# Kernel tuning notes

Measured on AMD Instinct MI355X. Metric: run time of the kernel, lower is better.

The kernel has to match this reference:

```python
import jax, jax.numpy as jnp
import numpy as np

B, N, D_IN, D_OUT, NHOP = 16, 1024, 128, 128, 3


def setup_inputs() -> dict:
    key = jax.random.key(0)
    ks = jax.random.split(key, 7)
    x = jax.random.normal(ks[0], (B, N, D_IN), dtype=jnp.float32)
    # sparse-ish binary adjacency (float, as in the torch model) with self loops
    adj = (jax.random.uniform(ks[1], (B, N, N)) < 0.05).astype(jnp.float32)
    adj = jnp.maximum(adj, jnp.eye(N, dtype=jnp.float32)[None])
    # learned params (torch nn.Linear default-ish init scale)
    s_in = 1.0 / np.sqrt(D_IN)
    s_out = 1.0 / np.sqrt(2 * D_OUT)
    W_w = jax.random.uniform(ks[2], (D_OUT, D_IN), minval=-s_in, maxval=s_in, dtype=jnp.float32)
    W_b = jax.random.uniform(ks[3], (D_OUT,), minval=-s_in, maxval=s_in, dtype=jnp.float32)
    A = jax.random.normal(ks[4], (D_OUT, D_OUT), dtype=jnp.float32) * 0.02  # nn.Parameter(zeros) would kill signal; use small init
    gate_w = jax.random.uniform(ks[5], (1, 2 * D_OUT), minval=-s_out, maxval=s_out, dtype=jnp.float32)
    gate_b = jax.random.uniform(ks[6], (1,), minval=-s_out, maxval=s_out, dtype=jnp.float32)
    return {"x": x, "adj": adj, "W_w": W_w, "W_b": W_b, "A": A,
            "gate_w": gate_w, "gate_b": gate_b}


def reference(x, adj, W_w, W_b, A, gate_w, gate_b):
    # h = W(x): [B,N,D_OUT]
    h = jnp.einsum('bnd,od->bno', x, W_w) + W_b
    # bilinear score e[b,j,k] = (h A)_j . h_k, symmetrized
    e = jnp.einsum('bjl,bkl->bjk', jnp.einsum('bjd,de->bje', h, A), h)
    e = e + jnp.swapaxes(e, 1, 2)
    # masked softmax over dim=1 (as in the torch code), then re-mask
    att = jnp.where(adj > 0, e, jnp.zeros((), dtype=e.dtype))
    att = jax.nn.softmax(att, axis=1)
    att = att * adj
    retval = h
    for _ in range(NHOP):
        az = jax.nn.relu(jnp.einsum('bij,bjk->bik', att, retval))
        gate_in = jnp.concatenate([h, az], axis=-1)            # [B,N,2*D_OUT]
        coeff = jax.nn.sigmoid(jnp.einsum('bnf,of->bno', gate_in, gate_w) + gate_b)  # [B,N,1]
        retval = coeff * h + (1.0 - coeff) * az
    return retval
```

## Files before the change

kernel.cpp:

```cpp
#include <hip/hip_runtime.h>
#include <math.h>

#define Bn 16
#define Nn 1024
#define Dn 128

typedef unsigned short ushort;
typedef unsigned long long u64;
typedef short short8 __attribute__((ext_vector_type(8)));
typedef float f32x4 __attribute__((ext_vector_type(4)));
typedef ushort us8 __attribute__((ext_vector_type(8)));
typedef ushort us4 __attribute__((ext_vector_type(4)));

__device__ __forceinline__ ushort f2bf(float f) {
    unsigned u = __float_as_uint(f);
    u += 0x7fff + ((u >> 16) & 1);
    return (ushort)(u >> 16);
}
__device__ __forceinline__ float bf2f(ushort s) {
    return __uint_as_float(((unsigned)s) << 16);
}

#if defined(__has_builtin)
#if __has_builtin(__builtin_amdgcn_global_load_lds)
#define HAVE_GLL 1
#endif
#endif
#ifndef HAVE_GLL
#define HAVE_GLL 0
#endif

typedef __attribute__((address_space(1))) void as1_t;
typedef __attribute__((address_space(3))) void as3_t;

__device__ __forceinline__ void stage_group(const void* gbase, void* lbase, int lane) {
#if HAVE_GLL
    __builtin_amdgcn_global_load_lds((as1_t*)((const char*)gbase + lane * 16),
                                     (as3_t*)lbase, 16, 0, 0);
#else
    *(us8*)((char*)lbase + lane * 16) = *(const us8*)((const char*)gbase + lane * 16);
#endif
}


__global__ __launch_bounds__(256) void k_ph0(const float* __restrict__ Ww,
                                             const float* __restrict__ A,
                                             const float* __restrict__ adj,
                                             ushort* __restrict__ Whi, ushort* __restrict__ Wlo,
                                             ushort* __restrict__ AThi, ushort* __restrict__ ATlo,
                                             float* __restrict__ Z, u64* __restrict__ bm) {
    int L = blockIdx.x, t = threadIdx.x;
    if (L < 64) {
        int i = L * 256 + t;
        float w = Ww[i];
        ushort wh = f2bf(w);
        Whi[i] = wh;
        Wlo[i] = f2bf(w - bf2f(wh));
        int e = i >> 7, d = i & 127;
        float a = A[d * Dn + e];
        ushort ah = f2bf(a);
        AThi[i] = ah;
        ATlo[i] = f2bf(a - bf2f(ah));
        Z[i] = (float)Nn;
    }
    int gwv = L * 4 + (t >> 6);
    int lane = t & 63;
    #pragma unroll 4
    for (int it = 0; it < 16; ++it) {
        int pair = gwv * 16 + it;
        const float* p = adj + (size_t)pair * 256 + lane * 4;
        float4 v = *(const float4*)p;
        u64 b0 = __ballot(v.x > 0.f);
        u64 b1 = __ballot(v.y > 0.f);
        u64 b2 = __ballot(v.z > 0.f);
        u64 b3 = __ballot(v.w > 0.f);
        if (lane == 0) {
            u64* d = bm + (size_t)pair * 4;
            d[0] = b0; d[1] = b1; d[2] = b2; d[3] = b3;
        }
    }
}

__global__ __launch_bounds__(256) void k_h(const float* __restrict__ x,
                                           const float* __restrict__ Wb,
                                           const ushort* __restrict__ Whi,
                                           const ushort* __restrict__ Wlo,
                                           const ushort* __restrict__ AThi,
                                           const ushort* __restrict__ ATlo,
                                           float* __restrict__ h,
                                           ushort* __restrict__ h16f,
                                           ushort* __restrict__ hA16f) {
    int I0 = blockIdx.x * 16;
    int t = threadIdx.x, w = t >> 6, lane = t & 63;
    int m = lane & 15, q = lane >> 4;

    __shared__ float xs[16][Dn + 4];
    __shared__ float hs[16][Dn + 4];
    __shared__ float has[16][Dn + 4];

    {
        int r = t >> 4, c8 = (t & 15) * 8;
        const float* src = x + (size_t)(I0 + r) * Dn + c8;
        *(float4*)&xs[r][c8]     = *(const float4*)(src);
        *(float4*)&xs[r][c8 + 4] = *(const float4*)(src + 4);
    }
    __syncthreads();

    f32x4 acc0 = {0,0,0,0}, acc1 = {0,0,0,0};
    #pragma unroll
    for (int ks = 0; ks < 4; ++ks) {
        int k0 = q * 8 + ks * 32;
        float v[8]; short8 ahi, alo;
        *(float4*)(v)     = *(const float4*)(&xs[m][k0]);
        *(float4*)(v + 4) = *(const float4*)(&xs[m][k0 + 4]);
        #pragma unroll
        for (int j = 0; j < 8; ++j) {
            ushort hi = f2bf(v[j]);
            ahi[j] = (short)hi;
            alo[j] = (short)f2bf(v[j] - bf2f(hi));
        }
        #pragma unroll
        for (int nn = 0; nn < 2; ++nn) {
            int brow = (w * 2 + nn) * 16 + m;
            short8 bhi = __builtin_bit_cast(short8, ((const us8*)(Whi + (size_t)brow * Dn))[q + ks * 4]);
            short8 blo = __builtin_bit_cast(short8, ((const us8*)(Wlo + (size_t)brow * Dn))[q + ks * 4]);
            f32x4 acc = nn ? acc1 : acc0;
            acc = __builtin_amdgcn_mfma_f32_16x16x32_bf16(ahi, bhi, acc, 0, 0, 0);
            acc = __builtin_amdgcn_mfma_f32_16x16x32_bf16(alo, bhi, acc, 0, 0, 0);
            acc = __builtin_amdgcn_mfma_f32_16x16x32_bf16(ahi, blo, acc, 0, 0, 0);
            if (nn) acc1 = acc; else acc0 = acc;
        }
    }
    #pragma unroll
    for (int nn = 0; nn < 2; ++nn) {
        int col = (w * 2 + nn) * 16 + m;
        float bias = Wb[col];
        f32x4 acc = nn ? acc1 : acc0;
        #pragma unroll
        for (int r = 0; r < 4; ++r) {
            int rl = q * 4 + r;
            float hv = acc[r] + bias;
            h[(size_t)(I0 + rl) * Dn + col] = hv;
            hs[rl][col] = hv;
        }
    }
    __syncthreads();

    f32x4 bcc0 = {0,0,0,0}, bcc1 = {0,0,0,0};
    #pragma unroll
    for (int ks = 0; ks < 4; ++ks) {
        int k0 = q * 8 + ks * 32;
        float v[8]; short8 ahi, alo;
        *(float4*)(v)     = *(const float4*)(&hs[m][k0]);
        *(float4*)(v + 4) = *(const float4*)(&hs[m][k0 + 4]);
        #pragma unroll
        for (int j = 0; j < 8; ++j) {
            ushort hi = f2bf(v[j]);
            ahi[j] = (short)hi;
            alo[j] = (short)f2bf(v[j] - bf2f(hi));
        }
        #pragma unroll
        for (int nn = 0; nn < 2; ++nn) {
            int brow = (w * 2 + nn) * 16 + m;
            short8 bhi = __builtin_bit_cast(short8, ((const us8*)(AThi + (size_t)brow * Dn))[q + ks * 4]);
            short8 blo = __builtin_bit_cast(short8, ((const us8*)(ATlo + (size_t)brow * Dn))[q + ks * 4]);
            f32x4 acc = nn ? bcc1 : bcc0;
            acc = __builtin_amdgcn_mfma_f32_16x16x32_bf16(ahi, bhi, acc, 0, 0, 0);
            acc = __builtin_amdgcn_mfma_f32_16x16x32_bf16(alo, bhi, acc, 0, 0, 0);
            acc = __builtin_amdgcn_mfma_f32_16x16x32_bf16(ahi, blo, acc, 0, 0, 0);
            if (nn) bcc1 = acc; else bcc0 = acc;
        }
    }
    #pragma unroll
    for (int nn = 0; nn < 2; ++nn) {
        int col = (w * 2 + nn) * 16 + m;
        f32x4 acc = nn ? bcc1 : bcc0;
        #pragma unroll
        for (int r = 0; r < 4; ++r)
            has[q * 4 + r][col] = acc[r];
    }
    __syncthreads();

    {
        int kc = t >> 6, mm = (t >> 2) & 15, qq = t & 3;
        int cb = kc * 32 + qq * 8;
        us8 oh, oa;
        #pragma unroll
        for (int e = 0; e < 8; ++e) {
            oh[e] = f2bf(hs[mm][cb + e]);
            oa[e] = f2bf(has[mm][cb + e]);
        }
        size_t U = (size_t)(I0 >> 4) * 256 + kc * 64 + mm * 4 + qq;
        ((us8*)h16f)[U]  = oh;
        ((us8*)hA16f)[U] = oa;
    }
}

__global__ __launch_bounds__(256, 2) void k_scores(const ushort* __restrict__ h16f,
                                                   const ushort* __restrict__ hA16f,
                                                   const u64* __restrict__ bm,
                                                   ushort* __restrict__ Ef,
                                                   float* __restrict__ Z) {
    int L = blockIdx.x;
    int b    = ((L & 7) << 1) | (L >> 11);
    int tile = (L >> 3) & 255;
    int I0 = (tile >> 4) << 6;
    int J0 = (tile & 15) << 6;
    int t = threadIdx.x, wid = t >> 6, lane = t & 63;
    int m = lane & 15, q = lane >> 4;

    __shared__ __align__(16) char smem[66560];
    float (*sc)[68] = (float(*)[68])smem;
    float (*cz)[64] = (float(*)[64])(smem + 65536);

    {
        const char* hb  = (const char*)h16f  + (size_t)b * 16384 * 16;
        const char* ab  = (const char*)hA16f + (size_t)b * 16384 * 16;
        for (int g = wid; g < 64; g += 4) {
            int arr = g >> 4, rt_l = (g >> 2) & 3, kk = g & 3;
            int rbase = ((arr < 2) ? (I0 >> 4) : (J0 >> 4)) + rt_l;
            const char* base = (arr & 1) ? ab : hb;
            const char* gp = base + ((size_t)rbase * 256 + kk * 64) * 16;
            stage_group(gp, smem + g * 1024, lane);
        }
    }
    __syncthreads();

    int off16 = (m * 4 + q) * 16;
    f32x4 acc[4] = {};
    #pragma unroll
    for (int ks = 0; ks < 4; ++ks) {
        short8 a1 = __builtin_bit_cast(short8, *(const us8*)(smem + 16384 + (wid * 4 + ks) * 1024 + off16));
        short8 a2 = __builtin_bit_cast(short8, *(const us8*)(smem +         (wid * 4 + ks) * 1024 + off16));
        #pragma unroll
        for (int nt = 0; nt < 4; ++nt) {
            short8 b1 = __builtin_bit_cast(short8, *(const us8*)(smem + 32768 + (nt * 4 + ks) * 1024 + off16));
            short8 b2 = __builtin_bit_cast(short8, *(const us8*)(smem + 49152 + (nt * 4 + ks) * 1024 + off16));
            acc[nt] = __builtin_amdgcn_mfma_f32_16x16x32_bf16(a1, b1, acc[nt], 0, 0, 0);
            acc[nt] = __builtin_amdgcn_mfma_f32_16x16x32_bf16(a2, b2, acc[nt], 0, 0, 0);
        }
    }
    __syncthreads();

    #pragma unroll
    for (int nt = 0; nt < 4; ++nt)
        #pragma unroll
        for (int r = 0; r < 4; ++r)
            sc[wid * 16 + q * 4 + r][nt * 16 + m] = acc[nt][r];
    __syncthreads();

    int row16 = t >> 4, c = t & 15;
    int bitc = ((J0 >> 2) & 63) + c;
    float colsum[4] = {0.f, 0.f, 0.f, 0.f};
    #pragma unroll
    for (int it = 0; it < 4; ++it) {
        int row = it * 16 + row16;
        const u64* wp = bm + ((size_t)(b * Nn + I0 + row) * 4 + (J0 >> 8)) * 4;
        u64 wj[4] = {wp[0], wp[1], wp[2], wp[3]};
        float s4[4];
        *(float4*)s4 = *(const float4*)(&sc[row][c * 4]);
        us4 e4;
        #pragma unroll
        for (int j = 0; j < 4; ++j) {
            float ex = __expf(s4[j]);
            bool on = (wj[j] >> bitc) & 1;
            e4[j] = f2bf(on ? ex : 0.f);
            colsum[j] += on ? (ex - 1.0f) : 0.f;
        }
        size_t U = ((((size_t)b * 64 + (I0 >> 4) + it) * 32 + (J0 >> 5) + (c >> 3)) * 16 + row16) * 4
                 + ((c & 7) >> 1);
        *(us4*)(Ef + U * 8 + (c & 1) * 4) = e4;
    }
    #pragma unroll
    for (int j = 0; j < 4; ++j) {
        colsum[j] += __shfl_xor(colsum[j], 16, 64);
        colsum[j] += __shfl_xor(colsum[j], 32, 64);
    }
    if (lane < 16) {
        #pragma unroll
        for (int j = 0; j < 4; ++j) cz[wid][lane * 4 + j] = colsum[j];
    }
    __syncthreads();
    if (t < 64) {
        float s = cz[0][t] + cz[1][t] + cz[2][t] + cz[3][t];
        atomicAdd(&Z[b * Nn + J0 + t], s);
    }
}

__global__ __launch_bounds__(256) void k_prep(const float* __restrict__ src,
                                              const float* __restrict__ Z,
                                              ushort* __restrict__ Tf) {
    int b = blockIdx.y;
    int j0 = blockIdx.x * 64;
    int t = threadIdx.x;
    __shared__ float ls[64][129];
    __shared__ float iz[64];
    if (t < 64) iz[t] = 1.0f / Z[b * Nn + j0 + t];
    __syncthreads();
    #pragma unroll
    for (int it = 0; it < 8; ++it) {
        int idx = it * 256 + t;
        int j = idx >> 5, k4 = (idx & 31) * 4;
        float4 v = *(const float4*)(src + ((size_t)b * Nn + j0 + j) * Dn + k4);
        float z = iz[j];
        ls[j][k4] = v.x * z; ls[j][k4 + 1] = v.y * z;
        ls[j][k4 + 2] = v.z * z; ls[j][k4 + 3] = v.w * z;
    }
    __syncthreads();
    int k = t & 127, half = t >> 7;
    us8 o[4];
    #pragma unroll
    for (int qq = 0; qq < 4; ++qq) {
        us8 tmp;
        #pragma unroll
        for (int e = 0; e < 8; ++e)
            tmp[e] = f2bf(ls[half * 32 + qq * 8 + e][k]);
        o[qq] = tmp;
    }
    size_t U = (((size_t)(k >> 4) * 32 + (j0 >> 5) + half) * 16 + (k & 15)) * 4;
    us8* dst = (us8*)(Tf + (size_t)b * 131072 + U * 8);
    dst[0] = o[0]; dst[1] = o[1]; dst[2] = o[2]; dst[3] = o[3];
}

__global__ __launch_bounds__(256) void k_hop(const ushort* __restrict__ Ef,
                                             const ushort* __restrict__ Tf,
                                             const float* __restrict__ h,
                                             const float* __restrict__ Z,
                                             const float* __restrict__ gw,
                                             const float* __restrict__ gb,
                                             ushort* __restrict__ Tfn,
                                             float* __restrict__ out,
                                             int last) {
    int L = blockIdx.x;
    int b  = ((L & 7) << 1) | (L >> 7);
    int t4 = (L >> 3) & 15;
    int t = threadIdx.x, w = t >> 6, lane = t & 63;
    int m = lane & 15, q = lane >> 4;
    int rt = t4 * 4 + w;
    int I0 = rt << 4;

    __shared__ __align__(16) char smem[49152];
    int off16 = (m * 4 + q) * 16;

    f32x4 acc[8] = {};
    for (int cch = 0; cch < 8; ++cch) {
        for (int g = w; g < 48; g += 4) {
            const char* gp; char* lp;
            if (g < 16) {
                int rr = g >> 2, kk = g & 3;
                gp = (const char*)Ef + ((((size_t)b * 64 + t4 * 4 + rr) * 32 + cch * 4 + kk) * 64) * 16;
                lp = smem + g * 1024;
            } else {
                int gb2 = g - 16, nt = gb2 >> 2, kk = gb2 & 3;
                gp = (const char*)Tf + ((((size_t)b * 8 + nt) * 32 + cch * 4 + kk) * 64) * 16;
                lp = smem + 16384 + gb2 * 1024;
            }
            stage_group(gp, lp, lane);
        }
        __syncthreads();

        #pragma unroll
        for (int kk = 0; kk < 4; ++kk) {
            short8 a = __builtin_bit_cast(short8, *(const us8*)(smem + (w * 4 + kk) * 1024 + off16));
            #pragma unroll
            for (int nt = 0; nt < 8; ++nt) {
                short8 bf = __builtin_bit_cast(short8,
                    *(const us8*)(smem + 16384 + (nt * 4 + kk) * 1024 + off16));
                acc[nt] = __builtin_amdgcn_mfma_f32_16x16x32_bf16(a, bf, acc[nt], 0, 0, 0);
            }
        }
        __syncthreads();
    }

    float gb0 = gb[0];
    float gwa[8], gwz[8];
    #pragma unroll
    for (int nt = 0; nt < 8; ++nt) { gwa[nt] = gw[nt * 16 + m]; gwz[nt] = gw[Dn + nt * 16 + m]; }

    float hv[8][4], coef[4];
    size_t hbase = ((size_t)b * Nn + I0) * Dn;
    #pragma unroll
    for (int r = 0; r < 4; ++r) {
        int row = q * 4 + r;
        float gs = 0.f;
        #pragma unroll
        for (int nt = 0; nt < 8; ++nt) {
            float az = fmaxf(acc[nt][r], 0.f);
            acc[nt][r] = az;
            float hh = h[hbase + (size_t)row * Dn + nt * 16 + m];
            hv[nt][r] = hh;
            gs += hh * gwa[nt] + az * gwz[nt];
        }
        gs += __shfl_xor(gs, 1, 64);
        gs += __shfl_xor(gs, 2, 64);
        gs += __shfl_xor(gs, 4, 64);
        gs += __shfl_xor(gs, 8, 64);
        coef[r] = 1.0f / (1.0f + __expf(-(gs + gb0)));
    }

    if (last) {
        #pragma unroll
        for (int r = 0; r < 4; ++r) {
            int row = q * 4 + r;
            float cc = coef[r];
            #pragma unroll
            for (int nt = 0; nt < 8; ++nt)
                out[hbase + (size_t)row * Dn + nt * 16 + m] =
                    cc * hv[nt][r] + (1.f - cc) * acc[nt][r];
        }
    } else {
        ushort (*tt)[128][16] = (ushort(*)[128][16])smem;
        #pragma unroll
        for (int r = 0; r < 4; ++r) {
            int row = q * 4 + r;
            float cc = coef[r];
            float iz = 1.0f / Z[b * Nn + I0 + row];
            #pragma unroll
            for (int nt = 0; nt < 8; ++nt) {
                float v = cc * hv[nt][r] + (1.f - cc) * acc[nt][r];
                tt[w][nt * 16 + m][row] = f2bf(v * iz);
            }
        }
        __syncthreads();
        int k = t >> 1, jh = t & 1;
        size_t U0 = (((size_t)(k >> 4) * 32 + t4 * 2 + jh) * 16 + (k & 15)) * 4;
        ushort* dst = Tfn + (size_t)b * 131072 + U0 * 8;
        #pragma unroll
        for (int qq = 0; qq < 4; ++qq)
            *(us8*)(dst + qq * 8) = *(const us8*)&tt[jh * 2 + (qq >> 1)][k][(qq & 1) * 8];
    }
}

extern "C" void kernel_launch(void* const* d_in, const int* in_sizes, int n_in,
                              void* d_out, int out_size, void* d_ws, size_t ws_size,
                              hipStream_t stream) {
    const float* x    = (const float*)d_in[0];
    const float* adj  = (const float*)d_in[1];
    const float* Ww   = (const float*)d_in[2];
    const float* Wb   = (const float*)d_in[3];
    const float* A    = (const float*)d_in[4];
    const float* gw   = (const float*)d_in[5];
    const float* gb   = (const float*)d_in[6];
    float* out = (float*)d_out;

    char* ws = (char*)d_ws;
    float*  h    = (float*)(ws);
    ushort* Ta   = (ushort*)(ws + (8u << 20));
    ushort* Tb   = (ushort*)(ws + (12u << 20));
    ushort* E    = (ushort*)(ws + (16u << 20));
    float*  Z    = (float*)(ws + (48u << 20));
    ushort* Whi  = (ushort*)(ws + (48u << 20) + (64u << 10));
    ushort* Wlo  = (ushort*)(ws + (48u << 20) + (96u << 10));
    ushort* AThi = (ushort*)(ws + (48u << 20) + (128u << 10));
    ushort* ATlo = (ushort*)(ws + (48u << 20) + (160u << 10));
    u64*    bm   = (u64*)(ws + (48u << 20) + (192u << 10));

    k_ph0   <<<1024, 256, 0, stream>>>(Ww, A, adj, Whi, Wlo, AThi, ATlo, Z, bm);
    k_h     <<<1024, 256, 0, stream>>>(x, Wb, Whi, Wlo, AThi, ATlo, h, Ta, Tb);
    k_scores<<<4096, 256, 0, stream>>>(Ta, Tb, bm, E, Z);
    k_prep  <<<dim3(16, Bn), 256, 0, stream>>>(h, Z, Ta);
    k_hop   <<<256, 256, 0, stream>>>(E, Ta, h, Z, gw, gb, Tb, out, 0);
    k_hop   <<<256, 256, 0, stream>>>(E, Tb, h, Z, gw, gb, Ta, out, 0);
    k_hop   <<<256, 256, 0, stream>>>(E, Ta, h, Z, gw, gb, (ushort*)nullptr, out, 1);
}
```

Baseline: 228.9 us.

## Shrink LDS in scores and split hop work across 1024 blocks

k_scores now loads the A-side (row) fragments straight from global memory into registers and stages only the column tiles in LDS. This halves shared memory so four blocks can fit per CU. k_hop is restructured so each block handles one 16-row tile, and its four waves split the 128 output columns instead of the rows. That raises the grid from 256 to 1024 blocks and fills the GPU better. The B operand (T) is now read directly from global memory without LDS staging, and the gate dot product is reduced across waves through shared memory. The cost is more redundant global reads of T across blocks and an extra block synchronisation for the gate reduction.

Result: no change. 231.6 us (+1.2%).

```diff
diff --git a/kernel.cpp b/kernel.cpp
--- a/kernel.cpp
+++ b/kernel.cpp
@@ -196,7 +196,7 @@
     }
 }
 
-__global__ __launch_bounds__(256, 2) void k_scores(const ushort* __restrict__ h16f,
+__global__ __launch_bounds__(256, 4) void k_scores(const ushort* __restrict__ h16f,
                                                    const ushort* __restrict__ hA16f,
                                                    const u64* __restrict__ bm,
                                                    ushort* __restrict__ Ef,
@@ -209,33 +209,44 @@
     int t = threadIdx.x, wid = t >> 6, lane = t & 63;
     int m = lane & 15, q = lane >> 4;
 
-    __shared__ __align__(16) char smem[66560];
+    __shared__ __align__(16) char smem[33792];
     float (*sc)[68] = (float(*)[68])smem;
-    float (*cz)[64] = (float(*)[64])(smem + 65536);
+    float (*cz)[64] = (float(*)[64])(smem + 32768);
 
     {
-        const char* hb  = (const char*)h16f  + (size_t)b * 16384 * 16;
-        const char* ab  = (const char*)hA16f + (size_t)b * 16384 * 16;
-        for (int g = wid; g < 64; g += 4) {
+        const char* hb = (const char*)h16f  + (size_t)b * 16384 * 16;
+        const char* ab = (const char*)hA16f + (size_t)b * 16384 * 16;
+        for (int g = wid; g < 32; g += 4) {
             int arr = g >> 4, rt_l = (g >> 2) & 3, kk = g & 3;
-            int rbase = ((arr < 2) ? (I0 >> 4) : (J0 >> 4)) + rt_l;
-            const char* base = (arr & 1) ? ab : hb;
+            int rbase = (J0 >> 4) + rt_l;
+            const char* base = arr ? ab : hb;
             const char* gp = base + ((size_t)rbase * 256 + kk * 64) * 16;
             stage_group(gp, smem + g * 1024, lane);
         }
     }
-    __syncthreads();
-
-    int off16 = (m * 4 + q) * 16;
+
+    const us8* Hf = (const us8*)h16f  + (size_t)b * 16384;
+    const us8* Af = (const us8*)hA16f + (size_t)b * 16384;
+    int off = m * 4 + q;
+    int rtA = (I0 >> 4) + wid;
+    us8 A1[4], A2[4];
+    #pragma unroll
+    for (int ks = 0; ks < 4; ++ks) {
+        A1[ks] = Af[rtA * 256 + ks * 64 + off];
+        A2[ks] = Hf[rtA * 256 + ks * 64 + off];
+    }
+    __syncthreads();
+
+    int off16 = off * 16;
     f32x4 acc[4] = {};
     #pragma unroll
     for (int ks = 0; ks < 4; ++ks) {
-        short8 a1 = __builtin_bit_cast(short8, *(const us8*)(smem + 16384 + (wid * 4 + ks) * 1024 + off16));
-        short8 a2 = __builtin_bit_cast(short8, *(const us8*)(smem +         (wid * 4 + ks) * 1024 + off16));
+        short8 a1 = __builtin_bit_cast(short8, A1[ks]);
+        short8 a2 = __builtin_bit_cast(short8, A2[ks]);
         #pragma unroll
         for (int nt = 0; nt < 4; ++nt) {
-            short8 b1 = __builtin_bit_cast(short8, *(const us8*)(smem + 32768 + (nt * 4 + ks) * 1024 + off16));
-            short8 b2 = __builtin_bit_cast(short8, *(const us8*)(smem + 49152 + (nt * 4 + ks) * 1024 + off16));
+            short8 b1 = __builtin_bit_cast(short8, *(const us8*)(smem +         (nt * 4 + ks) * 1024 + off16));
+            short8 b2 = __builtin_bit_cast(short8, *(const us8*)(smem + 16384 + (nt * 4 + ks) * 1024 + off16));
             acc[nt] = __builtin_amdgcn_mfma_f32_16x16x32_bf16(a1, b1, acc[nt], 0, 0, 0);
             acc[nt] = __builtin_amdgcn_mfma_f32_16x16x32_bf16(a2, b2, acc[nt], 0, 0, 0);
         }
@@ -322,112 +333,99 @@
     dst[0] = o[0]; dst[1] = o[1]; dst[2] = o[2]; dst[3] = o[3];
 }
 
-__global__ __launch_bounds__(256) void k_hop(const ushort* __restrict__ Ef,
-                                             const ushort* __restrict__ Tf,
-                                             const float* __restrict__ h,
-                                             const float* __restrict__ Z,
-                                             const float* __restrict__ gw,
-                                             const float* __restrict__ gb,
-                                             ushort* __restrict__ Tfn,
-                                             float* __restrict__ out,
-                                             int last) {
+__global__ __launch_bounds__(256, 4) void k_hop(const ushort* __restrict__ Ef,
+                                                const ushort* __restrict__ Tf,
+                                                const float* __restrict__ h,
+                                                const float* __restrict__ Z,
+                                                const float* __restrict__ gw,
+                                                const float* __restrict__ gb,
+                                                ushort* __restrict__ Tfn,
+                                                float* __restrict__ out,
+                                                int last) {
     int L = blockIdx.x;
-    int b  = ((L & 7) << 1) | (L >> 7);
-    int t4 = (L >> 3) & 15;
+    int b  = ((L & 7) << 1) | (L >> 9);
+    int rt = (L >> 3) & 63;
+    int I0 = rt << 4;
     int t = threadIdx.x, w = t >> 6, lane = t & 63;
     int m = lane & 15, q = lane >> 4;
-    int rt = t4 * 4 + w;
-    int I0 = rt << 4;
-
-    __shared__ __align__(16) char smem[49152];
-    int off16 = (m * 4 + q) * 16;
-
-    f32x4 acc[8] = {};
-    for (int cch = 0; cch < 8; ++cch) {
-        for (int g = w; g < 48; g += 4) {
-            const char* gp; char* lp;
-            if (g < 16) {
-                int rr = g >> 2, kk = g & 3;
-                gp = (const char*)Ef + ((((size_t)b * 64 + t4 * 4 + rr) * 32 + cch * 4 + kk) * 64) * 16;
-                lp = smem + g * 1024;
-            } else {
-                int gb2 = g - 16, nt = gb2 >> 2, kk = gb2 & 3;
-                gp = (const char*)Tf + ((((size_t)b * 8 + nt) * 32 + cch * 4 + kk) * 64) * 16;
-                lp = smem + 16384 + gb2 * 1024;
-            }
-            stage_group(gp, lp, lane);
-        }
-        __syncthreads();
-
-        #pragma unroll
-        for (int kk = 0; kk < 4; ++kk) {
-            short8 a = __builtin_bit_cast(short8, *(const us8*)(smem + (w * 4 + kk) * 1024 + off16));
-            #pragma unroll
-            for (int nt = 0; nt < 8; ++nt) {
-                short8 bf = __builtin_bit_cast(short8,
-                    *(const us8*)(smem + 16384 + (nt * 4 + kk) * 1024 + off16));
-                acc[nt] = __builtin_amdgcn_mfma_f32_16x16x32_bf16(a, bf, acc[nt], 0, 0, 0);
-            }
-        }
-        __syncthreads();
+
+    __shared__ __align__(16) char smem[33152];
+    float (*red)[16] = (float(*)[16])(smem + 32768);
+    float* cs = (float*)(smem + 32768 + 256);
+    float* zz = (float*)(smem + 32768 + 320);
+    ushort (*tt)[24] = (ushort(*)[24])smem;
+
+    {
+        const char* Eb = (const char*)Ef + ((size_t)b * 64 + rt) * 32768;
+        for (int g = w; g < 32; g += 4)
+            stage_group(Eb + g * 1024, smem + g * 1024, lane);
+    }
+
+    int off = m * 4 + q;
+    const us8* pB0 = (const us8*)Tf + ((size_t)b * 8 + 2 * w) * 2048 + off;
+    const us8* pB1 = pB0 + 2048;
+    __syncthreads();
+
+    const us8* As = (const us8*)smem;
+    f32x4 acc0 = {0,0,0,0}, acc1 = {0,0,0,0};
+    #pragma unroll 8
+    for (int kc = 0; kc < 32; ++kc) {
+        int o = kc * 64;
+        short8 a  = __builtin_bit_cast(short8, As[o + off]);
+        short8 b0 = __builtin_bit_cast(short8, pB0[o]);
+        short8 b1 = __builtin_bit_cast(short8, pB1[o]);
+        acc0 = __builtin_amdgcn_mfma_f32_16x16x32_bf16(a, b0, acc0, 0, 0, 0);
+        acc1 = __builtin_amdgcn_mfma_f32_16x16x32_bf16(a, b1, acc1, 0, 0, 0);
     }
 
     float gb0 = gb[0];
-    float gwa[8], gwz[8];
-    #pragma unroll
-    for (int nt = 0; nt < 8; ++nt) { gwa[nt] = gw[nt * 16 + m]; gwz[nt] = gw[Dn + nt * 16 + m]; }
-
-    float hv[8][4], coef[4];
+    int k0 = w * 32 + m, k1 = k0 + 16;
+    float g0a = gw[k0], g0z = gw[Dn + k0], g1a = gw[k1], g1z = gw[Dn + k1];
+    float hv0[4], hv1[4], az0[4], az1[4];
     size_t hbase = ((size_t)b * Nn + I0) * Dn;
     #pragma unroll
     for (int r = 0; r < 4; ++r) {
         int row = q * 4 + r;
-        float gs = 0.f;
-        #pragma unroll
-        for (int nt = 0; nt < 8; ++nt) {
-            float az = fmaxf(acc[nt][r], 0.f);
-            acc[nt][r] = az;
-            float hh = h[hbase + (size_t)row * Dn + nt * 16 + m];
-            hv[nt][r] = hh;
-            gs += hh * gwa[nt] + az * gwz[nt];
-        }
+        az0[r] = fmaxf(acc0[r], 0.f);
+        az1[r] = fmaxf(acc1[r], 0.f);
+        hv0[r] = h[hbase + (size_t)row * Dn + k0];
+        hv1[r] = h[hbase + (size_t)row * Dn + k1];
+        float gs = hv0[r] * g0a + az0[r] * g0z + hv1[r] * g1a + az1[r] * g1z;
         gs += __shfl_xor(gs, 1, 64);
         gs += __shfl_xor(gs, 2, 64);
         gs += __shfl_xor(gs, 4, 64);
         gs += __shfl_xor(gs, 8, 64);
-        coef[r] = 1.0f / (1.0f + __expf(-(gs + gb0)));
-    }
+        if (m == 0) red[w][row] = gs;
+    }
+    __syncthreads();
+    if (t < 16) {
+        float v = red[0][t] + red[1][t] + red[2][t] + red[3][t];
+        cs[t] = 1.0f / (1.0f + __expf(-(v + gb0)));
+        zz[t] = 1.0f / Z[b * Nn + I0 + t];
+    }
+    __syncthreads();
 
     if (last) {
         #pragma unroll
         for (int r = 0; r < 4; ++r) {
             int row = q * 4 + r;
-            float cc = coef[r];
-            #pragma unroll
-            for (int nt = 0; nt < 8; ++nt)
-                out[hbase + (size_t)row * Dn + nt * 16 + m] =
-                    cc * hv[nt][r] + (1.f - cc) * acc[nt][r];
+            float cc = cs[row];
+            out[hbase + (size_t)row * Dn + k0] = cc * hv0[r] + (1.f - cc) * az0[r];
+            out[hbase + (size_t)row * Dn + k1] = cc * hv1[r] + (1.f - cc) * az1[r];
         }
     } else {
-        ushort (*tt)[128][16] = (ushort(*)[128][16])smem;
         #pragma unroll
         for (int r = 0; r < 4; ++r) {
             int row = q * 4 + r;
-            float cc = coef[r];
-            float iz = 1.0f / Z[b * Nn + I0 + row];
-            #pragma unroll
-            for (int nt = 0; nt < 8; ++nt) {
-                float v = cc * hv[nt][r] + (1.f - cc) * acc[nt][r];
-                tt[w][nt * 16 + m][row] = f2bf(v * iz);
-            }
+            float cc = cs[row], iz = zz[row];
+            tt[k0][row] = f2bf((cc * hv0[r] + (1.f - cc) * az0[r]) * iz);
+            tt[k1][row] = f2bf((cc * hv1[r] + (1.f - cc) * az1[r]) * iz);
         }
         __syncthreads();
-        int k = t >> 1, jh = t & 1;
-        size_t U0 = (((size_t)(k >> 4) * 32 + t4 * 2 + jh) * 16 + (k & 15)) * 4;
-        ushort* dst = Tfn + (size_t)b * 131072 + U0 * 8;
-        #pragma unroll
-        for (int qq = 0; qq < 4; ++qq)
-            *(us8*)(dst + qq * 8) = *(const us8*)&tt[jh * 2 + (qq >> 1)][k][(qq & 1) * 8];
+        int k = t >> 1, part = t & 1;
+        size_t U = (((size_t)(k >> 4) * 32 + (I0 >> 5)) * 16 + (k & 15)) * 4
+                 + ((I0 & 31) >> 3) + part;
+        ((us8*)Tfn)[(size_t)b * 16384 + U] = *(const us8*)&tt[k][part * 8];
     }
 }
 
@@ -459,7 +457,7 @@
     k_h     <<<1024, 256, 0, stream>>>(x, Wb, Whi, Wlo, AThi, ATlo, h, Ta, Tb);
     k_scores<<<4096, 256, 0, stream>>>(Ta, Tb, bm, E, Z);
     k_prep  <<<dim3(16, Bn), 256, 0, stream>>>(h, Z, Ta);
-    k_hop   <<<256, 256, 0, stream>>>(E, Ta, h, Z, gw, gb, Tb, out, 0);
-    k_hop   <<<256, 256, 0, stream>>>(E, Tb, h, Z, gw, gb, Ta, out, 0);
-    k_hop   <<<256, 256, 0, stream>>>(E, Ta, h, Z, gw, gb, (ushort*)nullptr, out, 1);
-}
+    k_hop   <<<1024, 256, 0, stream>>>(E, Ta, h, Z, gw, gb, Tb, out, 0);
+    k_hop   <<<1024, 256, 0, stream>>>(E, Tb, h, Z, gw, gb, Ta, out, 0);
+    k_hop   <<<1024, 256, 0, stream>>>(E, Ta, h, Z, gw, gb, (ushort*)nullptr, out, 1);
+}
```
